# Optimization experiments

Hardware: AMD Instinct MI355X
Metric: run time of the kernel (lower is better)

## Reference

```python
import jax, jax.numpy as jnp
import numpy as np

N = 1024
H = 128


def setup_inputs() -> dict:
    key = jax.random.key(0)
    k1, k2, k3, k4, k5, k6 = jax.random.split(key, 6)
    s = 1.0 / np.sqrt(H)
    return {
        "node_feats": jax.random.normal(k1, (N, H), dtype=jnp.float32),
        "edge_attr": jax.random.normal(k2, (N * N, H), dtype=jnp.float32),
        "We": jax.random.uniform(k3, (H, H), jnp.float32, -s, s),
        "be": jax.random.uniform(k4, (H,), jnp.float32, -s, s),
        "Wi": jax.random.uniform(k5, (H, H), jnp.float32, -s, s),
        "Wj": jax.random.uniform(k6, (H, H), jnp.float32, -s, s),
    }


def reference(node_feats, edge_attr, We, be, Wi, Wj):
    # f_ij: [N^2, H] linear with bias
    f_ij = edge_attr @ We.T + be
    # f_i, f_j: [N, H] linears without bias
    f_i = node_feats @ Wi.T
    f_j = node_feats @ Wj.T
    # torch.matmul on 1-D vectors -> scalar dot; broadcast into each H-wide row.
    dots = jnp.einsum("ih,jh->ij", f_i, f_j)  # [N, N]
    fi_fj = dots.reshape(-1, 1)                 # [N^2, 1], broadcasts over H
    return jax.nn.relu(f_ij + fi_fj)
```

## Files before the change

kernel.cpp:

```cpp
#include <hip/hip_runtime.h>
#include <hip/hip_bf16.h>
#include <stdint.h>
#include <stddef.h>

typedef __bf16 bf16_t;
typedef __bf16 bf16x8 __attribute__((ext_vector_type(8)));
typedef float  f32x4  __attribute__((ext_vector_type(4)));

#define NN 1024
#define H  128
#define GRID 2048

__global__ void k_cvt_we(const float* __restrict__ src, bf16_t* __restrict__ dst) {
    int i = blockIdx.x * 256 + threadIdx.x;
    if (i < H * H) dst[i] = (bf16_t)src[i];
}

__global__ void k_proj(const float* __restrict__ node,
                       const float* __restrict__ Wi,
                       const float* __restrict__ Wj,
                       bf16_t* __restrict__ fi,
                       bf16_t* __restrict__ fj) {
    __shared__ float nrow[H];
    const int row = blockIdx.x;
    const int t   = threadIdx.x;
    const int h   = t & (H - 1);
    const int sel = t >> 7;
    if (t < H) nrow[t] = node[(size_t)row * H + t];
    __syncthreads();
    const float* w = (sel ? Wj : Wi) + (size_t)h * H;
    float acc = 0.f;
    #pragma unroll
    for (int k4 = 0; k4 < H / 4; ++k4) {
        f32x4 wv = *(const f32x4*)(w + k4 * 4);
        f32x4 nv = *(const f32x4*)(&nrow[k4 * 4]);
        acc += nv[0] * wv[0] + nv[1] * wv[1] + nv[2] * wv[2] + nv[3] * wv[3];
    }
    bf16_t* dst = sel ? fj : fi;
    dst[(size_t)row * H + h] = (bf16_t)acc;
}

__global__ __launch_bounds__(256, 4)
void k_dots(const bf16_t* __restrict__ fi,
            const bf16_t* __restrict__ fj,
            float* __restrict__ dots) {
    const int t    = threadIdx.x;
    const int wave = t >> 6;
    const int lane = t & 63;
    const int l15  = lane & 15;
    const int g    = lane >> 4;

    const int bm    = blockIdx.x >> 3;
    const int bn    = blockIdx.x & 7;
    const int ibase = bm * 64 + wave * 16;
    const int jbase = bn * 128;

    f32x4 acc[8];
    #pragma unroll
    for (int nt = 0; nt < 8; ++nt) acc[nt] = (f32x4){0.f, 0.f, 0.f, 0.f};

    const bf16_t* a = fi + (size_t)(ibase + l15) * H + g * 8;

    #pragma unroll
    for (int kst = 0; kst < 4; ++kst) {
        bf16x8 af = *(const bf16x8*)(a + kst * 32);
        #pragma unroll
        for (int nt = 0; nt < 8; ++nt) {
            bf16x8 bf = *(const bf16x8*)(fj + (size_t)(jbase + nt * 16 + l15) * H + kst * 32 + g * 8);
            acc[nt] = __builtin_amdgcn_mfma_f32_16x16x32_bf16(af, bf, acc[nt], 0, 0, 0);
        }
    }

    const int rbase = ibase + g * 4;
    #pragma unroll
    for (int r = 0; r < 4; ++r)
        #pragma unroll
        for (int nt = 0; nt < 8; ++nt)
            dots[(size_t)(rbase + r) * NN + jbase + nt * 16 + l15] = acc[nt][r];
}

__device__ __forceinline__ void gl_lds16(const float* g, float* l) {
    __builtin_amdgcn_global_load_lds(
        (const __attribute__((address_space(1))) unsigned int*)g,
        (__attribute__((address_space(3))) unsigned int*)l,
        16, 0, 0);
}

__global__ __launch_bounds__(256, 2)
void k_main(const float* __restrict__ edge,
            const bf16_t* __restrict__ web,
            const float* __restrict__ be,
            const float* __restrict__ dots,
            float* __restrict__ out) {
    __shared__ __align__(16) float bufA[64][H];
    __shared__ __align__(16) float bufB[64][H];
    __shared__ float lbias[H];

    const int t     = threadIdx.x;
    const int wave  = t >> 6;
    const int lane  = t & 63;
    const int l15   = lane & 15;
    const int g     = lane >> 4;
    const int lhalf = lane >> 5;
    const int b16   = (lane & 31) * 16;

    if (t < H) lbias[t] = be[t];
    __syncthreads();

    bf16x8 wfr[8][4];
    {
        const bf16_t* wp = web + (size_t)l15 * H + g * 8;
        #pragma unroll
        for (int nt = 0; nt < 8; ++nt)
            #pragma unroll
            for (int kk = 0; kk < 4; ++kk)
                wfr[nt][kk] = *(const bf16x8*)(wp + (size_t)(nt * 16) * H + kk * 32);
    }
    float dvv[8];
    #pragma unroll
    for (int k = 0; k < 8; ++k)
        dvv[k] = dots[(size_t)(blockIdx.x + k * GRID) * 64 + wave * 16 + l15];

    #pragma unroll
    for (int nt = 0; nt < 8; ++nt) {
        #pragma unroll
        for (int kk = 0; kk < 4; ++kk)
            asm volatile("" : "+v"(wfr[nt][kk]));
        asm volatile("" : "+v"(dvv[nt]));
    }

    #define STAGE(K, BUFP)                                                       \
        {                                                                        \
            const char* tb = (const char*)(edge + ((size_t)(blockIdx.x + (K) * GRID) * 64 + wave * 16) * H); \
            _Pragma("unroll")                                                    \
            for (int i = 0; i < 8; ++i) {                                        \
                const int r = 2 * i + lhalf;                                     \
                const int srcoff = r * 512 + (b16 ^ ((r & 7) << 4));             \
                gl_lds16((const float*)(tb + srcoff), &BUFP[wave * 16 + 2 * i][0]); \
            }                                                                    \
        }

    STAGE(0, bufA)

    const int sw = (l15 & 7) << 4;

    #pragma unroll
    for (int k = 0; k < 8; ++k) {
        if (k == 0) asm volatile("s_waitcnt vmcnt(0)" ::: "memory");
        else        asm volatile("s_waitcnt vmcnt(8)" ::: "memory");
        __builtin_amdgcn_sched_barrier(0);

        const char* lrow = (const char*)((k & 1) ? &bufB[0][0] : &bufA[0][0])
                         + (wave * 16 + l15) * 512;
        f32x4 u[8];
        #pragma unroll
        for (int kk = 0; kk < 4; ++kk) {
            u[2 * kk]     = *(const f32x4*)(lrow + kk * 128 + ((g * 32 +  0) ^ sw));
            u[2 * kk + 1] = *(const f32x4*)(lrow + kk * 128 + ((g * 32 + 16) ^ sw));
        }

        if (k < 7) {
            if (k & 1) { STAGE(k + 1, bufA) }
            else       { STAGE(k + 1, bufB) }
        }

        const float dv = dvv[k];
        f32x4 acc[8];
        #pragma unroll
        for (int nt = 0; nt < 8; ++nt) {
            f32x4 bv = *(const f32x4*)(&lbias[nt * 16 + g * 4]);
            #pragma unroll
            for (int r = 0; r < 4; ++r) acc[nt][r] = bv[r] + dv;
        }

        #pragma unroll
        for (int kk = 0; kk < 4; ++kk) {
            bf16x8 bfrag;
            #pragma unroll
            for (int i2 = 0; i2 < 4; ++i2) {
                bfrag[i2]     = (bf16_t)u[2 * kk][i2];
                bfrag[i2 + 4] = (bf16_t)u[2 * kk + 1][i2];
            }
            #pragma unroll
            for (int nt = 0; nt < 8; ++nt)
                acc[nt] = __builtin_amdgcn_mfma_f32_16x16x32_bf16(wfr[nt][kk], bfrag, acc[nt], 0, 0, 0);
        }

        float* op = out + ((size_t)(blockIdx.x + k * GRID) * 64 + wave * 16 + l15) * H + g * 4;
        #pragma unroll
        for (int nt = 0; nt < 8; ++nt) {
            f32x4 v;
            #pragma unroll
            for (int r = 0; r < 4; ++r) v[r] = fmaxf(acc[nt][r], 0.f);
            *(f32x4*)(op + nt * 16) = v;
        }
    }
    #undef STAGE
}

extern "C" void kernel_launch(void* const* d_in, const int* in_sizes, int n_in,
                              void* d_out, int out_size, void* d_ws, size_t ws_size,
                              hipStream_t stream) {
    const float* node = (const float*)d_in[0];
    const float* edge = (const float*)d_in[1];
    const float* We   = (const float*)d_in[2];
    const float* be   = (const float*)d_in[3];
    const float* Wi   = (const float*)d_in[4];
    const float* Wj   = (const float*)d_in[5];
    float* out = (float*)d_out;

    char* w = (char*)d_ws;
    bf16_t* fi_bf = (bf16_t*)w;
    bf16_t* fj_bf = (bf16_t*)(w + (256 << 10));
    float*  dots  = (float*)(w + (512 << 10));
    bf16_t* web   = (bf16_t*)(w + (512 << 10) + (4 << 20));

    k_cvt_we<<<(H * H + 255) / 256, 256, 0, stream>>>(We, web);
    k_proj<<<NN, 256, 0, stream>>>(node, Wi, Wj, fi_bf, fj_bf);
    k_dots<<<128, 256, 0, stream>>>(fi_bf, fj_bf, dots);
    k_main<<<GRID, 256, 0, stream>>>(edge, web, be, dots, out);
}
```

Baseline: 244.9 us.

## Restructure edge GEMM kernel to 32x32 MFMA tiles with contiguous per-block rows

The main kernel now runs 128-thread blocks that each own 512 contiguous edge rows, instead of rows strided across the grid. It switches from 16x16x32 to 32x32x16 bf16 MFMA with transposed operand roles, and loads the dots and bias values into LDS and registers. Outputs are written as scalar floats coalesced across 32 lanes instead of f32x4 vectors, and the vmcnt wait threshold is raised to account for the outstanding stores. The aim is better DRAM locality and fewer MFMA instructions per tile, at the cost of more store instructions and lower occupancy from the larger LDS footprint.

New measurement: 242.8 us. About the same (-0.9%).

```diff
diff --git a/kernel.cpp b/kernel.cpp
--- a/kernel.cpp
+++ b/kernel.cpp
@@ -6,6 +6,7 @@
 typedef __bf16 bf16_t;
 typedef __bf16 bf16x8 __attribute__((ext_vector_type(8)));
 typedef float  f32x4  __attribute__((ext_vector_type(4)));
+typedef float  f32x16 __attribute__((ext_vector_type(16)));
 
 #define NN 1024
 #define H  128
@@ -86,114 +87,112 @@
         16, 0, 0);
 }
 
-__global__ __launch_bounds__(256, 2)
+__global__ __launch_bounds__(128, 1)
 void k_main(const float* __restrict__ edge,
             const bf16_t* __restrict__ web,
             const float* __restrict__ be,
             const float* __restrict__ dots,
             float* __restrict__ out) {
-    __shared__ __align__(16) float bufA[64][H];
-    __shared__ __align__(16) float bufB[64][H];
-    __shared__ float lbias[H];
-
-    const int t     = threadIdx.x;
-    const int wave  = t >> 6;
-    const int lane  = t & 63;
-    const int l15   = lane & 15;
-    const int g     = lane >> 4;
-    const int lhalf = lane >> 5;
-    const int b16   = (lane & 31) * 16;
-
-    if (t < H) lbias[t] = be[t];
-    __syncthreads();
-
-    bf16x8 wfr[8][4];
+    __shared__ __align__(16) float ebuf[2][2][32][H];
+    __shared__ __align__(16) float dbuf[2][512];
+
+    const int t    = threadIdx.x;
+    const int wave = t >> 6;
+    const int lane = t & 63;
+    const int l31  = lane & 31;
+    const int h    = lane >> 5;
+    const size_t base = (size_t)blockIdx.x * 512;
+
+    bf16x8 wfr[4][8];
     {
-        const bf16_t* wp = web + (size_t)l15 * H + g * 8;
-        #pragma unroll
-        for (int nt = 0; nt < 8; ++nt)
-            #pragma unroll
-            for (int kk = 0; kk < 4; ++kk)
-                wfr[nt][kk] = *(const bf16x8*)(wp + (size_t)(nt * 16) * H + kk * 32);
-    }
-    float dvv[8];
-    #pragma unroll
-    for (int k = 0; k < 8; ++k)
-        dvv[k] = dots[(size_t)(blockIdx.x + k * GRID) * 64 + wave * 16 + l15];
-
-    #pragma unroll
-    for (int nt = 0; nt < 8; ++nt) {
-        #pragma unroll
-        for (int kk = 0; kk < 4; ++kk)
+        const bf16_t* wp = web + (size_t)l31 * H + h * 8;
+        #pragma unroll
+        for (int nt = 0; nt < 4; ++nt)
+            #pragma unroll
+            for (int kk = 0; kk < 8; ++kk)
+                wfr[nt][kk] = *(const bf16x8*)(wp + (size_t)(nt * 32) * H + kk * 16);
+    }
+    float bias[4];
+    #pragma unroll
+    for (int nt = 0; nt < 4; ++nt) bias[nt] = be[nt * 32 + l31];
+
+    #pragma unroll
+    for (int nt = 0; nt < 4; ++nt) {
+        #pragma unroll
+        for (int kk = 0; kk < 8; ++kk)
             asm volatile("" : "+v"(wfr[nt][kk]));
-        asm volatile("" : "+v"(dvv[nt]));
-    }
-
-    #define STAGE(K, BUFP)                                                       \
+        asm volatile("" : "+v"(bias[nt]));
+    }
+
+    gl_lds16(dots + base + lane * 4,       &dbuf[wave][0]);
+    gl_lds16(dots + base + 256 + lane * 4, &dbuf[wave][256]);
+
+    #define STAGE(K, BI)                                                         \
         {                                                                        \
-            const char* tb = (const char*)(edge + ((size_t)(blockIdx.x + (K) * GRID) * 64 + wave * 16) * H); \
+            const char* tb = (const char*)(edge + (base + (size_t)(K) * 64 + wave * 32) * H); \
             _Pragma("unroll")                                                    \
-            for (int i = 0; i < 8; ++i) {                                        \
-                const int r = 2 * i + lhalf;                                     \
-                const int srcoff = r * 512 + (b16 ^ ((r & 7) << 4));             \
-                gl_lds16((const float*)(tb + srcoff), &BUFP[wave * 16 + 2 * i][0]); \
+            for (int i = 0; i < 16; ++i) {                                       \
+                const int rr = 2 * i + h;                                        \
+                gl_lds16((const float*)(tb + rr * 512 + ((l31 * 16) ^ ((rr & 7) << 4))), \
+                         &ebuf[BI][wave][2 * i][0]);                             \
             }                                                                    \
         }
 
-    STAGE(0, bufA)
-
-    const int sw = (l15 & 7) << 4;
+    STAGE(0, 0)
+
+    const int sw = (l31 & 7) << 4;
 
     #pragma unroll
     for (int k = 0; k < 8; ++k) {
-        if (k == 0) asm volatile("s_waitcnt vmcnt(0)" ::: "memory");
-        else        asm volatile("s_waitcnt vmcnt(8)" ::: "memory");
+        if (k == 0) asm volatile("s_waitcnt vmcnt(0)"  ::: "memory");
+        else        asm volatile("s_waitcnt vmcnt(48)" ::: "memory");
         __builtin_amdgcn_sched_barrier(0);
 
-        const char* lrow = (const char*)((k & 1) ? &bufB[0][0] : &bufA[0][0])
-                         + (wave * 16 + l15) * 512;
-        f32x4 u[8];
-        #pragma unroll
-        for (int kk = 0; kk < 4; ++kk) {
-            u[2 * kk]     = *(const f32x4*)(lrow + kk * 128 + ((g * 32 +  0) ^ sw));
-            u[2 * kk + 1] = *(const f32x4*)(lrow + kk * 128 + ((g * 32 + 16) ^ sw));
+        const char* erow = (const char*)&ebuf[k & 1][wave][0][0] + l31 * 512;
+        f32x4 ua[8], ub[8];
+        #pragma unroll
+        for (int kk = 0; kk < 8; ++kk) {
+            ua[kk] = *(const f32x4*)(erow + ((kk * 64 + h * 32 +  0) ^ sw));
+            ub[kk] = *(const f32x4*)(erow + ((kk * 64 + h * 32 + 16) ^ sw));
         }
 
         if (k < 7) {
-            if (k & 1) { STAGE(k + 1, bufA) }
-            else       { STAGE(k + 1, bufB) }
-        }
-
-        const float dv = dvv[k];
-        f32x4 acc[8];
-        #pragma unroll
-        for (int nt = 0; nt < 8; ++nt) {
-            f32x4 bv = *(const f32x4*)(&lbias[nt * 16 + g * 4]);
-            #pragma unroll
-            for (int r = 0; r < 4; ++r) acc[nt][r] = bv[r] + dv;
-        }
-
-        #pragma unroll
-        for (int kk = 0; kk < 4; ++kk) {
-            bf16x8 bfrag;
-            #pragma unroll
-            for (int i2 = 0; i2 < 4; ++i2) {
-                bfrag[i2]     = (bf16_t)u[2 * kk][i2];
-                bfrag[i2 + 4] = (bf16_t)u[2 * kk + 1][i2];
+            if (k & 1) { STAGE(k + 1, 0) }
+            else       { STAGE(k + 1, 1) }
+        }
+
+        const float* dl = &dbuf[wave][k * 64 + wave * 32];
+        f32x4 dv[4];
+        #pragma unroll
+        for (int b = 0; b < 4; ++b)
+            dv[b] = *(const f32x4*)(dl + 4 * h + 8 * b);
+
+        f32x16 acc[4];
+        #pragma unroll
+        for (int nt = 0; nt < 4; ++nt)
+            #pragma unroll
+            for (int r = 0; r < 16; ++r)
+                acc[nt][r] = bias[nt] + dv[r >> 2][r & 3];
+
+        #pragma unroll
+        for (int kk = 0; kk < 8; ++kk) {
+            bf16x8 af;
+            #pragma unroll
+            for (int e = 0; e < 4; ++e) {
+                af[e]     = (bf16_t)ua[kk][e];
+                af[e + 4] = (bf16_t)ub[kk][e];
             }
             #pragma unroll
-            for (int nt = 0; nt < 8; ++nt)
-                acc[nt] = __builtin_amdgcn_mfma_f32_16x16x32_bf16(wfr[nt][kk], bfrag, acc[nt], 0, 0, 0);
-        }
-
-        float* op = out + ((size_t)(blockIdx.x + k * GRID) * 64 + wave * 16 + l15) * H + g * 4;
-        #pragma unroll
-        for (int nt = 0; nt < 8; ++nt) {
-            f32x4 v;
-            #pragma unroll
-            for (int r = 0; r < 4; ++r) v[r] = fmaxf(acc[nt][r], 0.f);
-            *(f32x4*)(op + nt * 16) = v;
-        }
+            for (int nt = 0; nt < 4; ++nt)
+                acc[nt] = __builtin_amdgcn_mfma_f32_32x32x16_bf16(af, wfr[nt][kk], acc[nt], 0, 0, 0);
+        }
+
+        float* orow = out + (base + (size_t)k * 64 + wave * 32 + 4 * h) * H + l31;
+        #pragma unroll
+        for (int nt = 0; nt < 4; ++nt)
+            #pragma unroll
+            for (int r = 0; r < 16; ++r)
+                orow[((r & 3) + 8 * (r >> 2)) * H + nt * 32] = fmaxf(acc[nt][r], 0.f);
     }
     #undef STAGE
 }
@@ -218,5 +217,5 @@
     k_cvt_we<<<(H * H + 255) / 256, 256, 0, stream>>>(We, web);
     k_proj<<<NN, 256, 0, stream>>>(node, Wi, Wj, fi_bf, fj_bf);
     k_dots<<<128, 256, 0, stream>>>(fi_bf, fj_bf, dots);
-    k_main<<<GRID, 256, 0, stream>>>(edge, web, be, dots, out);
-}
+    k_main<<<GRID, 128, 0, stream>>>(edge, web, be, dots, out);
+}
```
